# Optimization experiments

Measured on AMD Instinct MI355X. Metric: run time of the kernel, lower is better.

## Reference

```python
import jax, jax.numpy as jnp
import numpy as np

HID = 64  # hidden_dim


def _w(k, shape, fan):
    # torch default: U(-1/sqrt(hidden), 1/sqrt(hidden))
    bound = 1.0 / np.sqrt(fan)
    return jax.random.uniform(k, shape, jnp.float32, -bound, bound)


def setup_inputs() -> dict:
    key = jax.random.key(0)
    ks = jax.random.split(key, 16)
    B, L, S, D = 32, 168, 512, 1
    H = HID
    return {
        "x_seq": jax.random.normal(ks[0], (B, L, S, D), jnp.float32),
        # encoder LSTM layer 0 (input_size=D)
        "W_ih0": _w(ks[1], (4 * H, D), H), "W_hh0": _w(ks[2], (4 * H, H), H),
        "b_ih0": _w(ks[3], (4 * H,), H), "b_hh0": _w(ks[4], (4 * H,), H),
        # encoder LSTM layer 1 (input_size=H)
        "W_ih1": _w(ks[5], (4 * H, H), H), "W_hh1": _w(ks[6], (4 * H, H), H),
        "b_ih1": _w(ks[7], (4 * H,), H), "b_hh1": _w(ks[8], (4 * H,), H),
        # decoder LSTMCell (input_size=D)
        "Wc_ih": _w(ks[9], (4 * H, D), H), "Wc_hh": _w(ks[10], (4 * H, H), H),
        "bc_ih": _w(ks[11], (4 * H,), H), "bc_hh": _w(ks[12], (4 * H,), H),
        # output projection hidden -> input_dim
        "W_out": _w(ks[13], (D, H), H), "b_out": _w(ks[14], (D,), H),
        "horizon": 24,
    }


def _cell(x, h, c, Wih, Whh, bih, bhh):
    # torch gate order: i, f, g, o
    g = x @ Wih.T + bih + h @ Whh.T + bhh  # (N, 4H)
    i, f, gg, o = jnp.split(g, 4, axis=-1)
    c = jax.nn.sigmoid(f) * c + jax.nn.sigmoid(i) * jnp.tanh(gg)
    h = jax.nn.sigmoid(o) * jnp.tanh(c)
    return h, c


def _lstm_layer(x, Wih, Whh, bih, bhh):
    # x: (N, L, D_in) -> outputs (N, L, H), final h, c
    N = x.shape[0]
    Hd = Whh.shape[1]
    init = (jnp.zeros((N, Hd), x.dtype), jnp.zeros((N, Hd), x.dtype))

    def step(carry, xt):
        h, c = carry
        h, c = _cell(xt, h, c, Wih, Whh, bih, bhh)
        return (h, c), h

    (h, c), ys = jax.lax.scan(step, init, jnp.swapaxes(x, 0, 1))
    return jnp.swapaxes(ys, 0, 1), h, c


def reference(x_seq, W_ih0, W_hh0, b_ih0, b_hh0, W_ih1, W_hh1, b_ih1, b_hh1,
              Wc_ih, Wc_hh, bc_ih, bc_hh, W_out, b_out, horizon):
    B, L, S, D = x_seq.shape
    # (B, L, S, D) -> (B*S, L, D)
    x = jnp.transpose(x_seq, (0, 2, 1, 3)).reshape(B * S, L, D)
    # 2-layer encoder LSTM; dropout is identity in eval mode
    y1, _, _ = _lstm_layer(x, W_ih0, W_hh0, b_ih0, b_hh0)
    _, h, c = _lstm_layer(y1, W_ih1, W_hh1, b_ih1, b_hh1)
    x_cur = x[:, -1, :]

    def dec(carry, _):
        h, c, xc = carry
        h, c = _cell(xc, h, c, Wc_ih, Wc_hh, bc_ih, bc_hh)
        y = h @ W_out.T + b_out  # (N, D)
        return (h, c, y), y

    _, ys = jax.lax.scan(dec, (h, c, x_cur), None, length=horizon)  # (Hor, N, D)
    y = jnp.transpose(ys, (1, 0, 2)).reshape(B, S, horizon, D)
    return jnp.transpose(y, (0, 2, 1, 3))  # (B, Hor, S, D)
```

## Files before the change

### kernel.cpp

```cpp
#include <hip/hip_runtime.h>

typedef __attribute__((ext_vector_type(8))) short short8;
typedef __attribute__((ext_vector_type(4))) float f32x4;

#define MFMA16(a, b, c) __builtin_amdgcn_mfma_f32_16x16x32_bf16((a), (b), (c), 0, 0, 0)

constexpr int Bv  = 32;
constexpr int Lv  = 168;
constexpr int Sv  = 512;
constexpr int HZv = 24;
constexpr int Mv  = 32;
constexpr int HSTR = 88;
constexpr int HBUF = Mv * HSTR;
constexpr int PADv = 16000;

__device__ __forceinline__ float b2f(short s) {
    unsigned u = ((unsigned)(unsigned short)s) << 16;
    return __builtin_bit_cast(float, u);
}
__device__ __forceinline__ short f2b(float f) {
    unsigned u = __builtin_bit_cast(unsigned, f);
    unsigned r = (u + 0x7FFFu + ((u >> 16) & 1u)) >> 16;
    return (short)(unsigned short)r;
}
__device__ __forceinline__ float sigm(float x) {
    float e = __builtin_amdgcn_exp2f(-1.44269504088896f * x);
    return __builtin_amdgcn_rcpf(1.0f + e);
}
__device__ __forceinline__ float tanh_(float x) {
    float e = __builtin_amdgcn_exp2f(2.88539008177793f * x);
    return 1.0f - 2.0f * __builtin_amdgcn_rcpf(e + 1.0f);
}
__device__ __forceinline__ void hi8(const float* __restrict__ p, short8& hi) {
#pragma unroll
    for (int j = 0; j < 8; ++j) hi[j] = f2b(p[j]);
}

__global__ __launch_bounds__(256, 2)
void sitewise_lstm(const float* __restrict__ x_seq,
                   const float* __restrict__ Wih0, const float* __restrict__ Whh0,
                   const float* __restrict__ bih0, const float* __restrict__ bhh0,
                   const float* __restrict__ Wih1, const float* __restrict__ Whh1,
                   const float* __restrict__ bih1, const float* __restrict__ bhh1,
                   const float* __restrict__ Wcih, const float* __restrict__ Wchh,
                   const float* __restrict__ bcih, const float* __restrict__ bchh,
                   const float* __restrict__ Wout, const float* __restrict__ bout,
                   float* __restrict__ out)
{
    __shared__ __align__(16) short Hhi[4 * HBUF + PADv];
    __shared__ float woutF[64];
    __shared__ float ybufF[Mv];

    const int tid  = threadIdx.x;
    const int wv   = tid >> 6;
    const int lane = tid & 63;
    const int q    = lane >> 4;
    const int col  = lane & 15;
    const int U    = wv;
    const int bid  = blockIdx.x;
    const int b    = bid >> 4;
    const int s0   = (bid & 15) << 5;
    const int uu   = U * 16 + col;
    const int me   = q * 4;

    for (int i = tid; i < 4 * HBUF / 2; i += 256) ((int*)Hhi)[i] = 0;
    if (tid < 64) woutF[tid] = Wout[tid];

    const float* xbF = x_seq + b * Lv * Sv + s0;

    const int roA = col * HSTR + q * 8;
    const int wiA = me * HSTR + uu;

    short8 Whi[3][4][2];
    float bias0[4], bias1[4], biasc[4], wih0gE[4], wcihgE[4];
#pragma unroll
    for (int g = 0; g < 4; ++g) {
        const int j = g * 64 + uu;
        bias0[g] = bih0[j] + bhh0[j];
        bias1[g] = bih1[j] + bhh1[j];
        biasc[g] = bcih[j] + bchh[j];
#pragma unroll
        for (int kc = 0; kc < 2; ++kc) {
            const int off = j * 64 + kc * 32 + q * 8;
            hi8(Whh0 + off, Whi[0][g][kc]);
            hi8(Wih1 + off, Whi[1][g][kc]);
            hi8(Whh1 + off, Whi[2][g][kc]);
        }
        wih0gE[g] = Wih0[j];
        wcihgE[g] = Wcih[j];
    }

    float c0[8], c1[8];
#pragma unroll
    for (int i = 0; i < 8; ++i) { c0[i] = 0.f; c1[i] = 0.f; }

    __syncthreads();

#define ENC_STEP(T, B0P, B0N, B1P, B1N) do {                                          \
        f32x4 xv[2];                                                                  \
        xv[0] = *(const f32x4*)(xbF + (T) * Sv + me);                                 \
        xv[1] = *(const f32x4*)(xbF + (T) * Sv + me + 16);                            \
        short8 ah[2][2];                                                              \
        _Pragma("unroll")                                                             \
        for (int kc = 0; kc < 2; ++kc)                                                \
            _Pragma("unroll")                                                         \
            for (int mt = 0; mt < 2; ++mt)                                            \
                ah[kc][mt] = *(const short8*)(Hhi + (B0P) + roA + kc * 32 + mt * 16 * HSTR); \
        f32x4 pre0[4][2];                                                             \
        _Pragma("unroll")                                                             \
        for (int g = 0; g < 4; ++g)                                                   \
            _Pragma("unroll")                                                         \
            for (int mt = 0; mt < 2; ++mt)                                            \
                pre0[g][mt] = (f32x4){bias0[g], bias0[g], bias0[g], bias0[g]};        \
        _Pragma("unroll")                                                             \
        for (int g = 0; g < 4; ++g)                                                   \
            _Pragma("unroll")                                                         \
            for (int mt = 0; mt < 2; ++mt) pre0[g][mt] = MFMA16(ah[0][mt], Whi[0][g][0], pre0[g][mt]); \
        _Pragma("unroll")                                                             \
        for (int g = 0; g < 4; ++g)                                                   \
            _Pragma("unroll")                                                         \
            for (int mt = 0; mt < 2; ++mt) pre0[g][mt] = MFMA16(ah[1][mt], Whi[0][g][1], pre0[g][mt]); \
        _Pragma("unroll")                                                             \
        for (int mt = 0; mt < 2; ++mt)                                                \
            _Pragma("unroll")                                                         \
            for (int r = 0; r < 4; ++r) {                                             \
                const float xw = xv[mt][r];                                           \
                const float ig = sigm (pre0[0][mt][r] + xw * wih0gE[0]);              \
                const float fg = sigm (pre0[1][mt][r] + xw * wih0gE[1]);              \
                const float gt = tanh_(pre0[2][mt][r] + xw * wih0gE[2]);              \
                const float og = sigm (pre0[3][mt][r] + xw * wih0gE[3]);              \
                const float c  = fg * c0[mt * 4 + r] + ig * gt;                       \
                c0[mt * 4 + r] = c;                                                   \
                Hhi[(B0N) + wiA + (mt * 16 + r) * HSTR] = f2b(og * tanh_(c));         \
            }                                                                         \
        __syncthreads();                       \
        short8 bh[2][2], dh[2][2];                                                    \
        _Pragma("unroll")                                                             \
        for (int kc = 0; kc < 2; ++kc)                                                \
            _Pragma("unroll")                                                         \
            for (int mt = 0; mt < 2; ++mt) {                                          \
                bh[kc][mt] = *(const short8*)(Hhi + (B0N) + roA + kc * 32 + mt * 16 * HSTR); \
                dh[kc][mt] = *(const short8*)(Hhi + (B1P) + roA + kc * 32 + mt * 16 * HSTR); \
            }                                                                         \
        f32x4 pre1[4][2];                                                             \
        _Pragma("unroll")                                                             \
        for (int g = 0; g < 4; ++g)                                                   \
            _Pragma("unroll")                                                         \
            for (int mt = 0; mt < 2; ++mt)                                            \
                pre1[g][mt] = (f32x4){bias1[g], bias1[g], bias1[g], bias1[g]};        \
        _Pragma("unroll")                                                             \
        for (int g = 0; g < 4; ++g)                                                   \
            _Pragma("unroll")                                                         \
            for (int mt = 0; mt < 2; ++mt) pre1[g][mt] = MFMA16(bh[0][mt], Whi[1][g][0], pre1[g][mt]); \
        _Pragma("unroll")                                                             \
        for (int g = 0; g < 4; ++g)                                                   \
            _Pragma("unroll")                                                         \
            for (int mt = 0; mt < 2; ++mt) pre1[g][mt] = MFMA16(bh[1][mt], Whi[1][g][1], pre1[g][mt]); \
        _Pragma("unroll")                                                             \
        for (int g = 0; g < 4; ++g)                                                   \
            _Pragma("unroll")                                                         \
            for (int mt = 0; mt < 2; ++mt) pre1[g][mt] = MFMA16(dh[0][mt], Whi[2][g][0], pre1[g][mt]); \
        _Pragma("unroll")                                                             \
        for (int g = 0; g < 4; ++g)                                                   \
            _Pragma("unroll")                                                         \
            for (int mt = 0; mt < 2; ++mt) pre1[g][mt] = MFMA16(dh[1][mt], Whi[2][g][1], pre1[g][mt]); \
        _Pragma("unroll")                                                             \
        for (int mt = 0; mt < 2; ++mt)                                                \
            _Pragma("unroll")                                                         \
            for (int r = 0; r < 4; ++r) {                                             \
                const float ig = sigm (pre1[0][mt][r]);                               \
                const float fg = sigm (pre1[1][mt][r]);                               \
                const float gt = tanh_(pre1[2][mt][r]);                               \
                const float og = sigm (pre1[3][mt][r]);                               \
                const float c  = fg * c1[mt * 4 + r] + ig * gt;                       \
                c1[mt * 4 + r] = c;                                                   \
                Hhi[(B1N) + wiA + (mt * 16 + r) * HSTR] = f2b(og * tanh_(c));         \
            }                                                                         \
             \
             \
    } while (0)

    for (int t = 0; t < Lv; t += 2) {
        ENC_STEP(t,     0 * HBUF, 1 * HBUF, 2 * HBUF, 3 * HBUF);
        ENC_STEP(t + 1, 1 * HBUF, 0 * HBUF, 3 * HBUF, 2 * HBUF);
    }
#undef ENC_STEP

#pragma unroll
    for (int g = 0; g < 4; ++g)
#pragma unroll
        for (int kc = 0; kc < 2; ++kc)
            hi8(Wchh + (g * 64 + uu) * 64 + kc * 32 + q * 8, Whi[0][g][kc]);
    if (tid < Mv) ybufF[tid] = xbF[(Lv - 1) * Sv + tid];
    __syncthreads();

    const float boutF = bout[0];
    float* outp = out + b * HZv * Sv + s0;

#define DEC_STEP(T, B1P, B1N) do {                                                    \
        short8 ah[2][2];                                                              \
        _Pragma("unroll")                                                             \
        for (int kc = 0; kc < 2; ++kc)                                                \
            _Pragma("unroll")                                                         \
            for (int mt = 0; mt < 2; ++mt)                                            \
                ah[kc][mt] = *(const short8*)(Hhi + (B1P) + roA + kc * 32 + mt * 16 * HSTR); \
        float yv[2][4];                                                               \
        _Pragma("unroll")                                                             \
        for (int mt = 0; mt < 2; ++mt)                                                \
            _Pragma("unroll")                                                         \
            for (int r = 0; r < 4; ++r)                                               \
                yv[mt][r] = ybufF[me + mt * 16 + r];                                  \
        f32x4 prc[4][2];                                                              \
        _Pragma("unroll")                                                             \
        for (int g = 0; g < 4; ++g)                                                   \
            _Pragma("unroll")                                                         \
            for (int mt = 0; mt < 2; ++mt)                                            \
                prc[g][mt] = (f32x4){biasc[g], biasc[g], biasc[g], biasc[g]};         \
        _Pragma("unroll")                                                             \
        for (int g = 0; g < 4; ++g)                                                   \
            _Pragma("unroll")                                                         \
            for (int mt = 0; mt < 2; ++mt) prc[g][mt] = MFMA16(ah[0][mt], Whi[0][g][0], prc[g][mt]); \
        _Pragma("unroll")                                                             \
        for (int g = 0; g < 4; ++g)                                                   \
            _Pragma("unroll")                                                         \
            for (int mt = 0; mt < 2; ++mt) prc[g][mt] = MFMA16(ah[1][mt], Whi[0][g][1], prc[g][mt]); \
        _Pragma("unroll")                                                             \
        for (int mt = 0; mt < 2; ++mt)                                                \
            _Pragma("unroll")                                                         \
            for (int r = 0; r < 4; ++r) {                                             \
                const float xw = yv[mt][r];                                           \
                const float ig = sigm (prc[0][mt][r] + xw * wcihgE[0]);               \
                const float fg = sigm (prc[1][mt][r] + xw * wcihgE[1]);               \
                const float gt = tanh_(prc[2][mt][r] + xw * wcihgE[2]);               \
                const float og = sigm (prc[3][mt][r] + xw * wcihgE[3]);               \
                const float c  = fg * c1[mt * 4 + r] + ig * gt;                       \
                c1[mt * 4 + r] = c;                                                   \
                Hhi[(B1N) + wiA + (mt * 16 + r) * HSTR] = f2b(og * tanh_(c));         \
            }                                                                         \
        __syncthreads();                         \
        if (tid < 128) {        \
            const int m  = tid >> 2;                                                  \
            const int pp = tid & 3;                                                   \
            float s = 0.f;                                                            \
            _Pragma("unroll")                                                         \
            for (int k = 0; k < 16; ++k)                                              \
                s += b2f(Hhi[(B1N) + m * HSTR + pp * 16 + k]) * woutF[pp * 16 + k];   \
            s += __shfl_xor(s, 1, 64);                                                \
            s += __shfl_xor(s, 2, 64);                                                \
            if (pp == 0) {                                                            \
                const float y = s + boutF;                                            \
                outp[(T) * Sv + m] = y;                                               \
                ybufF[m] = y;                                                         \
            }                                                                         \
        }                                                                             \
        __syncthreads();                             \
    } while (0)

    for (int t = 0; t < HZv; t += 2) {
        DEC_STEP(t,     2 * HBUF, 3 * HBUF);
        DEC_STEP(t + 1, 3 * HBUF, 2 * HBUF);
    }
#undef DEC_STEP
}

extern "C" void kernel_launch(void* const* d_in, const int* in_sizes, int n_in,
                              void* d_out, int out_size, void* d_ws, size_t ws_size,
                              hipStream_t stream)
{
    const float* x_seq = (const float*)d_in[0];
    const float* Wih0  = (const float*)d_in[1];
    const float* Whh0  = (const float*)d_in[2];
    const float* bih0  = (const float*)d_in[3];
    const float* bhh0  = (const float*)d_in[4];
    const float* Wih1  = (const float*)d_in[5];
    const float* Whh1  = (const float*)d_in[6];
    const float* bih1  = (const float*)d_in[7];
    const float* bhh1  = (const float*)d_in[8];
    const float* Wcih  = (const float*)d_in[9];
    const float* Wchh  = (const float*)d_in[10];
    const float* bcih  = (const float*)d_in[11];
    const float* bchh  = (const float*)d_in[12];
    const float* Wout  = (const float*)d_in[13];
    const float* bout  = (const float*)d_in[14];
    float* out = (float*)d_out;

    hipLaunchKernelGGL(sitewise_lstm, dim3(Bv * (Sv / Mv)), dim3(256), 0, stream,
                       x_seq, Wih0, Whh0, bih0, bhh0, Wih1, Whh1, bih1, bhh1,
                       Wcih, Wchh, bcih, bchh, Wout, bout, out);
}
```

Measured before the change: 529.4 us.

## Halve sequences per block to 16 and raise occupancy to four blocks per CU

Each block now handles 16 site sequences instead of 32, so each wave issues one MFMA row tile per gate instead of two. The grid doubles to 1024 blocks, and launch bounds request 4 blocks per CU with a smaller LDS pad to fit. The goal is more concurrent blocks and waves to hide the serial recurrence latency across the 168+24 steps, at the cost of half the MFMA work per barrier and weights loaded by twice as many blocks.

```diff
diff --git a/kernel.cpp b/kernel.cpp
--- a/kernel.cpp
+++ b/kernel.cpp
@@ -9,10 +9,10 @@
 constexpr int Lv  = 168;
 constexpr int Sv  = 512;
 constexpr int HZv = 24;
-constexpr int Mv  = 32;
+constexpr int Mv  = 16;
 constexpr int HSTR = 88;
 constexpr int HBUF = Mv * HSTR;
-constexpr int PADv = 16000;
+constexpr int PADv = 13900;
 
 __device__ __forceinline__ float b2f(short s) {
     unsigned u = ((unsigned)(unsigned short)s) << 16;
@@ -36,7 +36,7 @@
     for (int j = 0; j < 8; ++j) hi[j] = f2b(p[j]);
 }
 
-__global__ __launch_bounds__(256, 2)
+__global__ __launch_bounds__(256, 4)
 void sitewise_lstm(const float* __restrict__ x_seq,
                    const float* __restrict__ Wih0, const float* __restrict__ Whh0,
                    const float* __restrict__ bih0, const float* __restrict__ bhh0,
@@ -58,8 +58,8 @@
     const int col  = lane & 15;
     const int U    = wv;
     const int bid  = blockIdx.x;
-    const int b    = bid >> 4;
-    const int s0   = (bid & 15) << 5;
+    const int b    = bid >> 5;
+    const int s0   = (bid & 31) << 4;
     const int uu   = U * 16 + col;
     const int me   = q * 4;
 
@@ -90,92 +90,66 @@
         wcihgE[g] = Wcih[j];
     }
 
-    float c0[8], c1[8];
-#pragma unroll
-    for (int i = 0; i < 8; ++i) { c0[i] = 0.f; c1[i] = 0.f; }
+    float c0[4], c1[4];
+#pragma unroll
+    for (int i = 0; i < 4; ++i) { c0[i] = 0.f; c1[i] = 0.f; }
 
     __syncthreads();
 
 #define ENC_STEP(T, B0P, B0N, B1P, B1N) do {                                          \
-        f32x4 xv[2];                                                                  \
-        xv[0] = *(const f32x4*)(xbF + (T) * Sv + me);                                 \
-        xv[1] = *(const f32x4*)(xbF + (T) * Sv + me + 16);                            \
-        short8 ah[2][2];                                                              \
+        f32x4 xv = *(const f32x4*)(xbF + (T) * Sv + me);                              \
+        short8 ah[2];                                                                 \
         _Pragma("unroll")                                                             \
         for (int kc = 0; kc < 2; ++kc)                                                \
-            _Pragma("unroll")                                                         \
-            for (int mt = 0; mt < 2; ++mt)                                            \
-                ah[kc][mt] = *(const short8*)(Hhi + (B0P) + roA + kc * 32 + mt * 16 * HSTR); \
-        f32x4 pre0[4][2];                                                             \
+            ah[kc] = *(const short8*)(Hhi + (B0P) + roA + kc * 32);                   \
+        f32x4 pre0[4];                                                                \
         _Pragma("unroll")                                                             \
         for (int g = 0; g < 4; ++g)                                                   \
-            _Pragma("unroll")                                                         \
-            for (int mt = 0; mt < 2; ++mt)                                            \
-                pre0[g][mt] = (f32x4){bias0[g], bias0[g], bias0[g], bias0[g]};        \
+            pre0[g] = (f32x4){bias0[g], bias0[g], bias0[g], bias0[g]};                \
+        _Pragma("unroll")                                                             \
+        for (int g = 0; g < 4; ++g) pre0[g] = MFMA16(ah[0], Whi[0][g][0], pre0[g]);   \
+        _Pragma("unroll")                                                             \
+        for (int g = 0; g < 4; ++g) pre0[g] = MFMA16(ah[1], Whi[0][g][1], pre0[g]);   \
+        _Pragma("unroll")                                                             \
+        for (int r = 0; r < 4; ++r) {                                                 \
+            const float xw = xv[r];                                                   \
+            const float ig = sigm (pre0[0][r] + xw * wih0gE[0]);                      \
+            const float fg = sigm (pre0[1][r] + xw * wih0gE[1]);                      \
+            const float gt = tanh_(pre0[2][r] + xw * wih0gE[2]);                      \
+            const float og = sigm (pre0[3][r] + xw * wih0gE[3]);                      \
+            const float c  = fg * c0[r] + ig * gt;                                    \
+            c0[r] = c;                                                                \
+            Hhi[(B0N) + wiA + r * HSTR] = f2b(og * tanh_(c));                         \
+        }                                                                             \
+        __syncthreads();                       \
+        short8 bh[2], dh[2];                                                          \
+        _Pragma("unroll")                                                             \
+        for (int kc = 0; kc < 2; ++kc) {                                              \
+            bh[kc] = *(const short8*)(Hhi + (B0N) + roA + kc * 32);                   \
+            dh[kc] = *(const short8*)(Hhi + (B1P) + roA + kc * 32);                   \
+        }                                                                             \
+        f32x4 pre1[4];                                                                \
         _Pragma("unroll")                                                             \
         for (int g = 0; g < 4; ++g)                                                   \
-            _Pragma("unroll")                                                         \
-            for (int mt = 0; mt < 2; ++mt) pre0[g][mt] = MFMA16(ah[0][mt], Whi[0][g][0], pre0[g][mt]); \
-        _Pragma("unroll")                                                             \
-        for (int g = 0; g < 4; ++g)                                                   \
-            _Pragma("unroll")                                                         \
-            for (int mt = 0; mt < 2; ++mt) pre0[g][mt] = MFMA16(ah[1][mt], Whi[0][g][1], pre0[g][mt]); \
-        _Pragma("unroll")                                                             \
-        for (int mt = 0; mt < 2; ++mt)                                                \
-            _Pragma("unroll")                                                         \
-            for (int r = 0; r < 4; ++r) {                                             \
-                const float xw = xv[mt][r];                                           \
-                const float ig = sigm (pre0[0][mt][r] + xw * wih0gE[0]);              \
-                const float fg = sigm (pre0[1][mt][r] + xw * wih0gE[1]);              \
-                const float gt = tanh_(pre0[2][mt][r] + xw * wih0gE[2]);              \
-                const float og = sigm (pre0[3][mt][r] + xw * wih0gE[3]);              \
-                const float c  = fg * c0[mt * 4 + r] + ig * gt;                       \
-                c0[mt * 4 + r] = c;                                                   \
-                Hhi[(B0N) + wiA + (mt * 16 + r) * HSTR] = f2b(og * tanh_(c));         \
-            }                                                                         \
-        __syncthreads();                       \
-        short8 bh[2][2], dh[2][2];                                                    \
-        _Pragma("unroll")                                                             \
-        for (int kc = 0; kc < 2; ++kc)                                                \
-            _Pragma("unroll")                                                         \
-            for (int mt = 0; mt < 2; ++mt) {                                          \
-                bh[kc][mt] = *(const short8*)(Hhi + (B0N) + roA + kc * 32 + mt * 16 * HSTR); \
-                dh[kc][mt] = *(const short8*)(Hhi + (B1P) + roA + kc * 32 + mt * 16 * HSTR); \
-            }                                                                         \
-        f32x4 pre1[4][2];                                                             \
-        _Pragma("unroll")                                                             \
-        for (int g = 0; g < 4; ++g)                                                   \
-            _Pragma("unroll")                                                         \
-            for (int mt = 0; mt < 2; ++mt)                                            \
-                pre1[g][mt] = (f32x4){bias1[g], bias1[g], bias1[g], bias1[g]};        \
-        _Pragma("unroll")                                                             \
-        for (int g = 0; g < 4; ++g)                                                   \
-            _Pragma("unroll")                                                         \
-            for (int mt = 0; mt < 2; ++mt) pre1[g][mt] = MFMA16(bh[0][mt], Whi[1][g][0], pre1[g][mt]); \
-        _Pragma("unroll")                                                             \
-        for (int g = 0; g < 4; ++g)                                                   \
-            _Pragma("unroll")                                                         \
-            for (int mt = 0; mt < 2; ++mt) pre1[g][mt] = MFMA16(bh[1][mt], Whi[1][g][1], pre1[g][mt]); \
-        _Pragma("unroll")                                                             \
-        for (int g = 0; g < 4; ++g)                                                   \
-            _Pragma("unroll")                                                         \
-            for (int mt = 0; mt < 2; ++mt) pre1[g][mt] = MFMA16(dh[0][mt], Whi[2][g][0], pre1[g][mt]); \
-        _Pragma("unroll")                                                             \
-        for (int g = 0; g < 4; ++g)                                                   \
-            _Pragma("unroll")                                                         \
-            for (int mt = 0; mt < 2; ++mt) pre1[g][mt] = MFMA16(dh[1][mt], Whi[2][g][1], pre1[g][mt]); \
-        _Pragma("unroll")                                                             \
-        for (int mt = 0; mt < 2; ++mt)                                                \
-            _Pragma("unroll")                                                         \
-            for (int r = 0; r < 4; ++r) {                                             \
-                const float ig = sigm (pre1[0][mt][r]);                               \
-                const float fg = sigm (pre1[1][mt][r]);                               \
-                const float gt = tanh_(pre1[2][mt][r]);                               \
-                const float og = sigm (pre1[3][mt][r]);                               \
-                const float c  = fg * c1[mt * 4 + r] + ig * gt;                       \
-                c1[mt * 4 + r] = c;                                                   \
-                Hhi[(B1N) + wiA + (mt * 16 + r) * HSTR] = f2b(og * tanh_(c));         \
-            }                                                                         \
+            pre1[g] = (f32x4){bias1[g], bias1[g], bias1[g], bias1[g]};                \
+        _Pragma("unroll")                                                             \
+        for (int g = 0; g < 4; ++g) pre1[g] = MFMA16(bh[0], Whi[1][g][0], pre1[g]);   \
+        _Pragma("unroll")                                                             \
+        for (int g = 0; g < 4; ++g) pre1[g] = MFMA16(bh[1], Whi[1][g][1], pre1[g]);   \
+        _Pragma("unroll")                                                             \
+        for (int g = 0; g < 4; ++g) pre1[g] = MFMA16(dh[0], Whi[2][g][0], pre1[g]);   \
+        _Pragma("unroll")                                                             \
+        for (int g = 0; g < 4; ++g) pre1[g] = MFMA16(dh[1], Whi[2][g][1], pre1[g]);   \
+        _Pragma("unroll")                                                             \
+        for (int r = 0; r < 4; ++r) {                                                 \
+            const float ig = sigm (pre1[0][r]);                                       \
+            const float fg = sigm (pre1[1][r]);                                       \
+            const float gt = tanh_(pre1[2][r]);                                       \
+            const float og = sigm (pre1[3][r]);                                       \
+            const float c  = fg * c1[r] + ig * gt;                                    \
+            c1[r] = c;                                                                \
+            Hhi[(B1N) + wiA + r * HSTR] = f2b(og * tanh_(c));                         \
+        }                                                                             \
              \
              \
     } while (0)
@@ -198,47 +172,35 @@
     float* outp = out + b * HZv * Sv + s0;
 
 #define DEC_STEP(T, B1P, B1N) do {                                                    \
-        short8 ah[2][2];                                                              \
+        short8 ah[2];                                                                 \
         _Pragma("unroll")                                                             \
         for (int kc = 0; kc < 2; ++kc)                                                \
-            _Pragma("unroll")                                                         \
-            for (int mt = 0; mt < 2; ++mt)                                            \
-                ah[kc][mt] = *(const short8*)(Hhi + (B1P) + roA + kc * 32 + mt * 16 * HSTR); \
-        float yv[2][4];                                                               \
-        _Pragma("unroll")                                                             \
-        for (int mt = 0; mt < 2; ++mt)                                                \
-            _Pragma("unroll")                                                         \
-            for (int r = 0; r < 4; ++r)                                               \
-                yv[mt][r] = ybufF[me + mt * 16 + r];                                  \
-        f32x4 prc[4][2];                                                              \
+            ah[kc] = *(const short8*)(Hhi + (B1P) + roA + kc * 32);                   \
+        float yv[4];                                                                  \
+        _Pragma("unroll")                                                             \
+        for (int r = 0; r < 4; ++r)                                                   \
+            yv[r] = ybufF[me + r];                                                    \
+        f32x4 prc[4];                                                                 \
         _Pragma("unroll")                                                             \
         for (int g = 0; g < 4; ++g)                                                   \
-            _Pragma("unroll")                                                         \
-            for (int mt = 0; mt < 2; ++mt)                                            \
-                prc[g][mt] = (f32x4){biasc[g], biasc[g], biasc[g], biasc[g]};         \
-        _Pragma("unroll")                                                             \
-        for (int g = 0; g < 4; ++g)                                                   \
-            _Pragma("unroll")                                                         \
-            for (int mt = 0; mt < 2; ++mt) prc[g][mt] = MFMA16(ah[0][mt], Whi[0][g][0], prc[g][mt]); \
-        _Pragma("unroll")                                                             \
-        for (int g = 0; g < 4; ++g)                                                   \
-            _Pragma("unroll")                                                         \
-            for (int mt = 0; mt < 2; ++mt) prc[g][mt] = MFMA16(ah[1][mt], Whi[0][g][1], prc[g][mt]); \
-        _Pragma("unroll")                                                             \
-        for (int mt = 0; mt < 2; ++mt)                                                \
-            _Pragma("unroll")                                                         \
-            for (int r = 0; r < 4; ++r) {                                             \
-                const float xw = yv[mt][r];                                           \
-                const float ig = sigm (prc[0][mt][r] + xw * wcihgE[0]);               \
-                const float fg = sigm (prc[1][mt][r] + xw * wcihgE[1]);               \
-                const float gt = tanh_(prc[2][mt][r] + xw * wcihgE[2]);               \
-                const float og = sigm (prc[3][mt][r] + xw * wcihgE[3]);               \
-                const float c  = fg * c1[mt * 4 + r] + ig * gt;                       \
-                c1[mt * 4 + r] = c;                                                   \
-                Hhi[(B1N) + wiA + (mt * 16 + r) * HSTR] = f2b(og * tanh_(c));         \
-            }                                                                         \
+            prc[g] = (f32x4){biasc[g], biasc[g], biasc[g], biasc[g]};                 \
+        _Pragma("unroll")                                                             \
+        for (int g = 0; g < 4; ++g) prc[g] = MFMA16(ah[0], Whi[0][g][0], prc[g]);     \
+        _Pragma("unroll")                                                             \
+        for (int g = 0; g < 4; ++g) prc[g] = MFMA16(ah[1], Whi[0][g][1], prc[g]);     \
+        _Pragma("unroll")                                                             \
+        for (int r = 0; r < 4; ++r) {                                                 \
+            const float xw = yv[r];                                                   \
+            const float ig = sigm (prc[0][r] + xw * wcihgE[0]);                       \
+            const float fg = sigm (prc[1][r] + xw * wcihgE[1]);                       \
+            const float gt = tanh_(prc[2][r] + xw * wcihgE[2]);                       \
+            const float og = sigm (prc[3][r] + xw * wcihgE[3]);                       \
+            const float c  = fg * c1[r] + ig * gt;                                    \
+            c1[r] = c;                                                                \
+            Hhi[(B1N) + wiA + r * HSTR] = f2b(og * tanh_(c));                         \
+        }                                                                             \
         __syncthreads();                         \
-        if (tid < 128) {        \
+        if (tid < 64) {            \
             const int m  = tid >> 2;                                                  \
             const int pp = tid & 3;                                                   \
             float s = 0.f;                                                            \
```

Measured after the change: 1.284 ms. 143% more time.
